# Kernel tuning notes

Measured on AMD Instinct MI355X. Metric: run time of the kernel, lower is better.

The kernel has to match this reference:

```python
import jax, jax.numpy as jnp
import numpy as np


def setup_inputs() -> dict:
    key = jax.random.key(0)
    k1, k2, k3, k4 = jax.random.split(key, 4)
    B, T, D, H = 512, 256, 512, 1024
    x = jax.random.normal(k1, (B, T, D), dtype=jnp.float32)
    # Glorot-ish scaling to keep tanh out of full saturation
    W = jax.random.normal(k2, (D, H), dtype=jnp.float32) / np.sqrt(D)
    U = jax.random.normal(k3, (H, H), dtype=jnp.float32) / np.sqrt(H)
    b = jnp.zeros((H,), dtype=jnp.float32)
    Wd = jax.random.normal(k4, (H, 1), dtype=jnp.float32) / np.sqrt(H)
    bd = jnp.zeros((1,), dtype=jnp.float32)
    return {"x": x, "W": W, "U": U, "b": b, "Wd": Wd, "bd": bd}


def reference(x, W, U, b, Wd, bd):
    # SimpleRNN: h_t = tanh(x_t @ W + h_{t-1} @ U + b), zero initial state.
    B, T, D = x.shape
    H = U.shape[0]
    # Precompute input projections for all timesteps in one big GEMM.
    xw = jnp.einsum('btd,dh->bth', x, W) + b  # [B, T, H]

    def step(h, xw_t):
        h_new = jnp.tanh(xw_t + h @ U)
        return h_new, None

    h0 = jnp.zeros((B, H), dtype=x.dtype)
    h_last, _ = jax.lax.scan(step, h0, jnp.swapaxes(xw, 0, 1))  # scan over T
    # Dense(1) on the last hidden state
    logits = h_last @ Wd + bd  # [B, 1]
    return logits
```

## Files before the change

kernel.cpp:

```cpp
#include <hip/hip_runtime.h>
#include <hip/hip_fp16.h>

#define NB 512
#define NTT 256
#define ND 512
#define NH 1024
#define NK 1536

typedef _Float16 f16;
typedef f16 f16x8 __attribute__((ext_vector_type(8)));
typedef f16 f16x4 __attribute__((ext_vector_type(4)));
typedef float f32x4 __attribute__((ext_vector_type(4)));

union U16x8 { unsigned long long q[2]; f16x8 v; uint4 u4; };
union U16x4 { unsigned long long q; f16x4 v; };

#define BAR_BYTES 4096
#define WUT_OFF  BAR_BYTES
#define WUT_BYTES (NH * NK * 2)
#define H_OFF    (WUT_OFF + WUT_BYTES)
#define H_BYTES  (2 * NB * NH * 2)

__global__ void prep_wut(const float* __restrict__ W, const float* __restrict__ U,
                         f16* __restrict__ WUT) {
    __shared__ float tile[64][65];
    int bk = blockIdx.x % 24, bn = blockIdx.x / 24;
    int k0 = bk * 64, n0 = bn * 64;
    int tid = threadIdx.x, jn = tid & 63;
#pragma unroll
    for (int p = 0; p < 16; ++p) {
        int kr = p * 4 + (tid >> 6);
        int k = k0 + kr;
        float v = (k < ND) ? W[(size_t)k * NH + n0 + jn] : U[(size_t)(k - ND) * NH + n0 + jn];
        tile[kr][jn] = v;
    }
    __syncthreads();
#pragma unroll
    for (int p = 0; p < 16; ++p) {
        int nr = p * 4 + (tid >> 6);
        int kc = tid & 63;
        WUT[(size_t)(n0 + nr) * NK + k0 + kc] = (f16)tile[kc][nr];
    }
}

__device__ __forceinline__ float fast_tanh(float x) {
    float e = __expf(-2.0f * x);
    return 2.0f / (1.0f + e) - 1.0f;
}

__global__ void __launch_bounds__(512, 1)
rnn4(const float* __restrict__ x, const f16* __restrict__ WUT,
     const float* __restrict__ bias, const float* __restrict__ Wd,
     const float* __restrict__ bd, f16* __restrict__ h,
     unsigned* __restrict__ bar, float* __restrict__ out) {
    __shared__ float red[4][64][36];
    __shared__ f16 trans[32][72];

    const int bid = blockIdx.x, tid = threadIdx.x;
    const int lane = tid & 63, wid = tid >> 6;
    const int lrow = lane & 15, lq = lane >> 4;
    const int xcd = bid & 7, m8 = bid >> 3;
    const int cl = xcd * 2 + (m8 >> 4);
    const int mem = m8 & 15;
    const int r0 = cl * 32, c0 = mem * 64;
    const int kx0 = wid * 64;
    const int kh0 = wid * 128;
    unsigned* cnt = bar + cl * 32;

    const int ec = wid * 8 + (lane & 7);
    const int eq = lane >> 3;
    const float bias_e = bias[c0 + ec];

    const int srow = tid >> 4, sseg = tid & 15;

    f16x8 bw[4][6];
#pragma unroll
    for (int j = 0; j < 4; ++j) {
        const int col = c0 + j * 16 + lrow;
        const f16* wp = WUT + (size_t)col * NK;
#pragma unroll
        for (int kt = 0; kt < 2; ++kt)
            bw[j][kt] = *(const f16x8*)(wp + kx0 + kt * 32 + lq * 8);
#pragma unroll
        for (int kt = 0; kt < 4; ++kt)
            bw[j][2 + kt] = *(const f16x8*)(wp + ND + kh0 + kt * 32 + lq * 8);
    }

    float4 xf[2][2][2];
#pragma unroll
    for (int m = 0; m < 2; ++m) {
        const float* xp = x + (size_t)(r0 + m * 16 + lrow) * (NTT * ND)
                            + kx0 + lq * 8;
#pragma unroll
        for (int kt = 0; kt < 2; ++kt) {
            xf[m][kt][0] = *(const float4*)(xp + kt * 32);
            xf[m][kt][1] = *(const float4*)(xp + kt * 32 + 4);
        }
    }

    for (int t = 0; t < NTT; ++t) {
        const f16* hprev = h + (size_t)(t & 1) * (NB * NH);
        f16* hnew = h + (size_t)((t + 1) & 1) * (NB * NH);

        f16x8 ax[2][2];
#pragma unroll
        for (int m = 0; m < 2; ++m)
#pragma unroll
            for (int kt = 0; kt < 2; ++kt) {
                const float4 a = xf[m][kt][0], b = xf[m][kt][1];
                f16x8 v = {(f16)a.x, (f16)a.y, (f16)a.z, (f16)a.w,
                           (f16)b.x, (f16)b.y, (f16)b.z, (f16)b.w};
                ax[m][kt] = v;
            }

        f32x4 acc[2][4] = {};
#pragma unroll
        for (int kt = 0; kt < 2; ++kt)
#pragma unroll
            for (int m = 0; m < 2; ++m)
#pragma unroll
                for (int j = 0; j < 4; ++j)
                    acc[m][j] = __builtin_amdgcn_mfma_f32_16x16x32_f16(ax[m][kt], bw[j][kt], acc[m][j], 0, 0, 0);

        {
            const unsigned want = (unsigned)t;
            while (__hip_atomic_load(cnt + 2 * wid,     __ATOMIC_RELAXED, __HIP_MEMORY_SCOPE_AGENT) < want ||
                   __hip_atomic_load(cnt + 2 * wid + 1, __ATOMIC_RELAXED, __HIP_MEMORY_SCOPE_AGENT) < want)
                __builtin_amdgcn_s_sleep(1);
            __builtin_amdgcn_sched_barrier(0);
        }

#pragma unroll
        for (int kt = 0; kt < 4; ++kt) {
            U16x8 a0, a1;
            const f16* p0 = hprev + (size_t)(r0 + lrow) * NH + kh0 + kt * 32 + lq * 8;
            const f16* p1 = p0 + (size_t)16 * NH;
            a0.q[0] = __hip_atomic_load((const unsigned long long*)p0, __ATOMIC_RELAXED, __HIP_MEMORY_SCOPE_AGENT);
            a0.q[1] = __hip_atomic_load((const unsigned long long*)p0 + 1, __ATOMIC_RELAXED, __HIP_MEMORY_SCOPE_AGENT);
            a1.q[0] = __hip_atomic_load((const unsigned long long*)p1, __ATOMIC_RELAXED, __HIP_MEMORY_SCOPE_AGENT);
            a1.q[1] = __hip_atomic_load((const unsigned long long*)p1 + 1, __ATOMIC_RELAXED, __HIP_MEMORY_SCOPE_AGENT);
#pragma unroll
            for (int j = 0; j < 4; ++j) {
                acc[0][j] = __builtin_amdgcn_mfma_f32_16x16x32_f16(a0.v, bw[j][2 + kt], acc[0][j], 0, 0, 0);
                acc[1][j] = __builtin_amdgcn_mfma_f32_16x16x32_f16(a1.v, bw[j][2 + kt], acc[1][j], 0, 0, 0);
            }
        }

        const int tn = (t + 1 < NTT) ? t + 1 : NTT - 1;
#pragma unroll
        for (int m = 0; m < 2; ++m) {
            const float* xp = x + (size_t)(r0 + m * 16 + lrow) * (NTT * ND)
                                + (size_t)tn * ND + kx0 + lq * 8;
#pragma unroll
            for (int kt = 0; kt < 2; ++kt) {
                xf[m][kt][0] = *(const float4*)(xp + kt * 32);
                xf[m][kt][1] = *(const float4*)(xp + kt * 32 + 4);
            }
        }

#define ST_PARTIAL(B)                                                          \
        {                                                                      \
            _Pragma("unroll")                                                  \
            for (int m = 0; m < 2; ++m)                                        \
                _Pragma("unroll")                                              \
                for (int j = 0; j < 4; ++j)                                    \
                    *(f32x4*)&red[B][j * 16 + lrow][m * 16 + lq * 4] = acc[m][j]; \
        }
#define ADD_PARTIAL(B)                                                         \
        {                                                                      \
            _Pragma("unroll")                                                  \
            for (int m = 0; m < 2; ++m)                                        \
                _Pragma("unroll")                                              \
                for (int j = 0; j < 4; ++j)                                    \
                    acc[m][j] += *(const f32x4*)&red[B][j * 16 + lrow][m * 16 + lq * 4]; \
        }
        if (wid >= 4) ST_PARTIAL(wid - 4);
        __syncthreads();
        if (wid < 4) {
            ADD_PARTIAL(wid);
            ST_PARTIAL(wid);
        }
        __syncthreads();

        {
            f32x4 s = *(const f32x4*)&red[0][ec][eq * 4];
#pragma unroll
            for (int b = 1; b < 4; ++b)
                s += *(const f32x4*)&red[b][ec][eq * 4];
#pragma unroll
            for (int r = 0; r < 4; ++r)
                trans[eq * 4 + r][ec] = (f16)fast_tanh(s[r] + bias_e);
        }
        __syncthreads();

        {
            U16x4 u;
            u.v = *(const f16x4*)&trans[srow][sseg * 4];
            __hip_atomic_store((unsigned long long*)(hnew + (size_t)(r0 + srow) * NH + c0 + sseg * 4),
                               u.q, __ATOMIC_RELAXED, __HIP_MEMORY_SCOPE_AGENT);
        }

        __syncthreads();
        if (tid == 0)
            __hip_atomic_store(cnt + mem, (unsigned)(t + 1), __ATOMIC_RELAXED, __HIP_MEMORY_SCOPE_AGENT);
    }

    if (mem == 0) {
        if (tid < 16) {
            while (__hip_atomic_load(cnt + tid, __ATOMIC_RELAXED, __HIP_MEMORY_SCOPE_AGENT) < (unsigned)NTT)
                __builtin_amdgcn_s_sleep(1);
        }
        __syncthreads();
        __builtin_amdgcn_sched_barrier(0);

        const f16* hlast = h;
        const int r = tid >> 4, seg = tid & 15;
        const f16* hp = hlast + (size_t)(r0 + r) * NH + seg * 64;
        const float* wp = Wd + seg * 64;
        float s = 0.f;
#pragma unroll
        for (int i = 0; i < 64; i += 8) {
            U16x8 u;
            u.q[0] = __hip_atomic_load((const unsigned long long*)(hp + i), __ATOMIC_RELAXED, __HIP_MEMORY_SCOPE_AGENT);
            u.q[1] = __hip_atomic_load((const unsigned long long*)(hp + i) + 1, __ATOMIC_RELAXED, __HIP_MEMORY_SCOPE_AGENT);
            const float4 w0 = *(const float4*)(wp + i);
            const float4 w1 = *(const float4*)(wp + i + 4);
            s += (float)u.v[0] * w0.x + (float)u.v[1] * w0.y +
                 (float)u.v[2] * w0.z + (float)u.v[3] * w0.w +
                 (float)u.v[4] * w1.x + (float)u.v[5] * w1.y +
                 (float)u.v[6] * w1.z + (float)u.v[7] * w1.w;
        }
        s += __shfl_xor(s, 1); s += __shfl_xor(s, 2);
        s += __shfl_xor(s, 4); s += __shfl_xor(s, 8);
        if (seg == 0) out[r0 + r] = s + bd[0];
    }
}

extern "C" void kernel_launch(void* const* d_in, const int* in_sizes, int n_in,
                              void* d_out, int out_size, void* d_ws, size_t ws_size,
                              hipStream_t stream) {
    const float* x  = (const float*)d_in[0];
    const float* W  = (const float*)d_in[1];
    const float* U  = (const float*)d_in[2];
    const float* b  = (const float*)d_in[3];
    const float* Wd = (const float*)d_in[4];
    const float* bd = (const float*)d_in[5];
    float* out = (float*)d_out;

    char* ws = (char*)d_ws;
    unsigned* bar = (unsigned*)ws;
    f16* WUT = (f16*)(ws + WUT_OFF);
    f16* h   = (f16*)(ws + H_OFF);

    hipMemsetAsync(bar, 0, BAR_BYTES, stream);
    hipMemsetAsync(h, 0, NB * NH * 2, stream);
    prep_wut<<<dim3(384), dim3(256), 0, stream>>>(W, U, WUT);

    void* args[8] = {(void*)&x, (void*)&WUT, (void*)&b, (void*)&Wd,
                     (void*)&bd, (void*)&h, (void*)&bar, (void*)&out};
    hipError_t err = hipLaunchCooperativeKernel(
        reinterpret_cast<const void*>(&rnn4), dim3(256), dim3(512), args, 0, stream);
    if (err != hipSuccess) {
        rnn4<<<dim3(256), dim3(512), 0, stream>>>(x, WUT, b, Wd, bd, h, bar, out);
    }
}
```

Before: 2.007 ms.

## Split each timestep into two 16-row halves with separate sync flags

```diff
diff --git a/kernel.cpp b/kernel.cpp
--- a/kernel.cpp
+++ b/kernel.cpp
@@ -13,7 +13,6 @@
 typedef float f32x4 __attribute__((ext_vector_type(4)));
 
 union U16x8 { unsigned long long q[2]; f16x8 v; uint4 u4; };
-union U16x4 { unsigned long long q; f16x4 v; };
 
 #define BAR_BYTES 4096
 #define WUT_OFF  BAR_BYTES
@@ -49,12 +48,12 @@
 }
 
 __global__ void __launch_bounds__(512, 1)
-rnn4(const float* __restrict__ x, const f16* __restrict__ WUT,
+rnn5(const float* __restrict__ x, const f16* __restrict__ WUT,
      const float* __restrict__ bias, const float* __restrict__ Wd,
      const float* __restrict__ bd, f16* __restrict__ h,
      unsigned* __restrict__ bar, float* __restrict__ out) {
-    __shared__ float red[4][64][36];
-    __shared__ f16 trans[32][72];
+    __shared__ float red[8][64][21];
+    __shared__ f16 trans[16][72];
 
     const int bid = blockIdx.x, tid = threadIdx.x;
     const int lane = tid & 63, wid = tid >> 6;
@@ -65,13 +64,13 @@
     const int r0 = cl * 32, c0 = mem * 64;
     const int kx0 = wid * 64;
     const int kh0 = wid * 128;
-    unsigned* cnt = bar + cl * 32;
-
-    const int ec = wid * 8 + (lane & 7);
-    const int eq = lane >> 3;
+    unsigned* flg = bar + cl * 64;
+
+    const int ec = tid & 63;
+    const int er = (tid >> 6) * 2;
     const float bias_e = bias[c0 + ec];
 
-    const int srow = tid >> 4, sseg = tid & 15;
+    const int srow = tid >> 5, sseg = tid & 31;
 
     f16x8 bw[4][6];
 #pragma unroll
@@ -88,127 +87,102 @@
 
     float4 xf[2][2][2];
 #pragma unroll
-    for (int m = 0; m < 2; ++m) {
-        const float* xp = x + (size_t)(r0 + m * 16 + lrow) * (NTT * ND)
+    for (int c = 0; c < 2; ++c) {
+        const float* xp = x + (size_t)(r0 + c * 16 + lrow) * (NTT * ND)
                             + kx0 + lq * 8;
 #pragma unroll
         for (int kt = 0; kt < 2; ++kt) {
-            xf[m][kt][0] = *(const float4*)(xp + kt * 32);
-            xf[m][kt][1] = *(const float4*)(xp + kt * 32 + 4);
+            xf[c][kt][0] = *(const float4*)(xp + kt * 32);
+            xf[c][kt][1] = *(const float4*)(xp + kt * 32 + 4);
         }
     }
 
     for (int t = 0; t < NTT; ++t) {
         const f16* hprev = h + (size_t)(t & 1) * (NB * NH);
         f16* hnew = h + (size_t)((t + 1) & 1) * (NB * NH);
-
-        f16x8 ax[2][2];
-#pragma unroll
-        for (int m = 0; m < 2; ++m)
+        const int tn = (t + 1 < NTT) ? t + 1 : NTT - 1;
+
+#pragma unroll
+        for (int c = 0; c < 2; ++c) {
+            unsigned* f = flg + c * 32;
+
+            f16x8 ax[2];
 #pragma unroll
             for (int kt = 0; kt < 2; ++kt) {
-                const float4 a = xf[m][kt][0], b = xf[m][kt][1];
+                const float4 a = xf[c][kt][0], b = xf[c][kt][1];
                 f16x8 v = {(f16)a.x, (f16)a.y, (f16)a.z, (f16)a.w,
                            (f16)b.x, (f16)b.y, (f16)b.z, (f16)b.w};
-                ax[m][kt] = v;
-            }
-
-        f32x4 acc[2][4] = {};
-#pragma unroll
-        for (int kt = 0; kt < 2; ++kt)
-#pragma unroll
-            for (int m = 0; m < 2; ++m)
+                ax[kt] = v;
+            }
+
+            f32x4 acc[4] = {};
+#pragma unroll
+            for (int kt = 0; kt < 2; ++kt)
 #pragma unroll
                 for (int j = 0; j < 4; ++j)
-                    acc[m][j] = __builtin_amdgcn_mfma_f32_16x16x32_f16(ax[m][kt], bw[j][kt], acc[m][j], 0, 0, 0);
-
-        {
-            const unsigned want = (unsigned)t;
-            while (__hip_atomic_load(cnt + 2 * wid,     __ATOMIC_RELAXED, __HIP_MEMORY_SCOPE_AGENT) < want ||
-                   __hip_atomic_load(cnt + 2 * wid + 1, __ATOMIC_RELAXED, __HIP_MEMORY_SCOPE_AGENT) < want)
-                __builtin_amdgcn_s_sleep(1);
-            __builtin_amdgcn_sched_barrier(0);
-        }
-
-#pragma unroll
-        for (int kt = 0; kt < 4; ++kt) {
-            U16x8 a0, a1;
-            const f16* p0 = hprev + (size_t)(r0 + lrow) * NH + kh0 + kt * 32 + lq * 8;
-            const f16* p1 = p0 + (size_t)16 * NH;
-            a0.q[0] = __hip_atomic_load((const unsigned long long*)p0, __ATOMIC_RELAXED, __HIP_MEMORY_SCOPE_AGENT);
-            a0.q[1] = __hip_atomic_load((const unsigned long long*)p0 + 1, __ATOMIC_RELAXED, __HIP_MEMORY_SCOPE_AGENT);
-            a1.q[0] = __hip_atomic_load((const unsigned long long*)p1, __ATOMIC_RELAXED, __HIP_MEMORY_SCOPE_AGENT);
-            a1.q[1] = __hip_atomic_load((const unsigned long long*)p1 + 1, __ATOMIC_RELAXED, __HIP_MEMORY_SCOPE_AGENT);
-#pragma unroll
-            for (int j = 0; j < 4; ++j) {
-                acc[0][j] = __builtin_amdgcn_mfma_f32_16x16x32_f16(a0.v, bw[j][2 + kt], acc[0][j], 0, 0, 0);
-                acc[1][j] = __builtin_amdgcn_mfma_f32_16x16x32_f16(a1.v, bw[j][2 + kt], acc[1][j], 0, 0, 0);
-            }
-        }
-
-        const int tn = (t + 1 < NTT) ? t + 1 : NTT - 1;
-#pragma unroll
-        for (int m = 0; m < 2; ++m) {
-            const float* xp = x + (size_t)(r0 + m * 16 + lrow) * (NTT * ND)
-                                + (size_t)tn * ND + kx0 + lq * 8;
-#pragma unroll
-            for (int kt = 0; kt < 2; ++kt) {
-                xf[m][kt][0] = *(const float4*)(xp + kt * 32);
-                xf[m][kt][1] = *(const float4*)(xp + kt * 32 + 4);
-            }
-        }
-
-#define ST_PARTIAL(B)                                                          \
-        {                                                                      \
-            _Pragma("unroll")                                                  \
-            for (int m = 0; m < 2; ++m)                                        \
-                _Pragma("unroll")                                              \
-                for (int j = 0; j < 4; ++j)                                    \
-                    *(f32x4*)&red[B][j * 16 + lrow][m * 16 + lq * 4] = acc[m][j]; \
-        }
-#define ADD_PARTIAL(B)                                                         \
-        {                                                                      \
-            _Pragma("unroll")                                                  \
-            for (int m = 0; m < 2; ++m)                                        \
-                _Pragma("unroll")                                              \
-                for (int j = 0; j < 4; ++j)                                    \
-                    acc[m][j] += *(const f32x4*)&red[B][j * 16 + lrow][m * 16 + lq * 4]; \
-        }
-        if (wid >= 4) ST_PARTIAL(wid - 4);
-        __syncthreads();
-        if (wid < 4) {
-            ADD_PARTIAL(wid);
-            ST_PARTIAL(wid);
-        }
-        __syncthreads();
-
-        {
-            f32x4 s = *(const f32x4*)&red[0][ec][eq * 4];
-#pragma unroll
-            for (int b = 1; b < 4; ++b)
-                s += *(const f32x4*)&red[b][ec][eq * 4];
-#pragma unroll
-            for (int r = 0; r < 4; ++r)
-                trans[eq * 4 + r][ec] = (f16)fast_tanh(s[r] + bias_e);
-        }
-        __syncthreads();
-
-        {
-            U16x4 u;
-            u.v = *(const f16x4*)&trans[srow][sseg * 4];
-            __hip_atomic_store((unsigned long long*)(hnew + (size_t)(r0 + srow) * NH + c0 + sseg * 4),
-                               u.q, __ATOMIC_RELAXED, __HIP_MEMORY_SCOPE_AGENT);
-        }
-
-        __syncthreads();
-        if (tid == 0)
-            __hip_atomic_store(cnt + mem, (unsigned)(t + 1), __ATOMIC_RELAXED, __HIP_MEMORY_SCOPE_AGENT);
+                    acc[j] = __builtin_amdgcn_mfma_f32_16x16x32_f16(ax[kt], bw[j][kt], acc[j], 0, 0, 0);
+
+            {
+                const unsigned want = (unsigned)t;
+                while (__hip_atomic_load(f + 2 * wid,     __ATOMIC_RELAXED, __HIP_MEMORY_SCOPE_AGENT) < want ||
+                       __hip_atomic_load(f + 2 * wid + 1, __ATOMIC_RELAXED, __HIP_MEMORY_SCOPE_AGENT) < want) {}
+                __builtin_amdgcn_sched_barrier(0);
+            }
+
+#pragma unroll
+            for (int kt = 0; kt < 4; ++kt) {
+                U16x8 a0;
+                const f16* p0 = hprev + (size_t)(r0 + c * 16 + lrow) * NH + kh0 + kt * 32 + lq * 8;
+                a0.q[0] = __hip_atomic_load((const unsigned long long*)p0, __ATOMIC_RELAXED, __HIP_MEMORY_SCOPE_AGENT);
+                a0.q[1] = __hip_atomic_load((const unsigned long long*)p0 + 1, __ATOMIC_RELAXED, __HIP_MEMORY_SCOPE_AGENT);
+#pragma unroll
+                for (int j = 0; j < 4; ++j)
+                    acc[j] = __builtin_amdgcn_mfma_f32_16x16x32_f16(a0.v, bw[j][2 + kt], acc[j], 0, 0, 0);
+            }
+
+            {
+                const float* xp = x + (size_t)(r0 + c * 16 + lrow) * (NTT * ND)
+                                    + (size_t)tn * ND + kx0 + lq * 8;
+#pragma unroll
+                for (int kt = 0; kt < 2; ++kt) {
+                    xf[c][kt][0] = *(const float4*)(xp + kt * 32);
+                    xf[c][kt][1] = *(const float4*)(xp + kt * 32 + 4);
+                }
+            }
+
+#pragma unroll
+            for (int j = 0; j < 4; ++j)
+                *(f32x4*)&red[wid][j * 16 + lrow][lq * 4] = acc[j];
+            __syncthreads();
+
+            {
+                float s0 = 0.f, s1 = 0.f;
+#pragma unroll
+                for (int b = 0; b < 8; ++b) {
+                    const float2 v = *(const float2*)&red[b][ec][er];
+                    s0 += v.x; s1 += v.y;
+                }
+                trans[er][ec]     = (f16)fast_tanh(s0 + bias_e);
+                trans[er + 1][ec] = (f16)fast_tanh(s1 + bias_e);
+            }
+            __syncthreads();
+
+            {
+                const unsigned uval = *(const unsigned*)&trans[srow][sseg * 2];
+                __hip_atomic_store((unsigned*)(hnew + (size_t)(r0 + c * 16 + srow) * NH + c0 + sseg * 2),
+                                   uval, __ATOMIC_RELAXED, __HIP_MEMORY_SCOPE_AGENT);
+            }
+
+            __syncthreads();
+            if (tid == 0)
+                __hip_atomic_store(f + mem, (unsigned)(t + 1), __ATOMIC_RELAXED, __HIP_MEMORY_SCOPE_AGENT);
+        }
     }
 
     if (mem == 0) {
-        if (tid < 16) {
-            while (__hip_atomic_load(cnt + tid, __ATOMIC_RELAXED, __HIP_MEMORY_SCOPE_AGENT) < (unsigned)NTT)
-                __builtin_amdgcn_s_sleep(1);
+        if (tid < 32) {
+            unsigned* fp = flg + (tid >> 4) * 32 + (tid & 15);
+            while (__hip_atomic_load(fp, __ATOMIC_RELAXED, __HIP_MEMORY_SCOPE_AGENT) < (unsigned)NTT) {}
         }
         __syncthreads();
         __builtin_amdgcn_sched_barrier(0);
@@ -259,8 +233,8 @@
     void* args[8] = {(void*)&x, (void*)&WUT, (void*)&b, (void*)&Wd,
                      (void*)&bd, (void*)&h, (void*)&bar, (void*)&out};
     hipError_t err = hipLaunchCooperativeKernel(
-        reinterpret_cast<const void*>(&rnn4), dim3(256), dim3(512), args, 0, stream);
+        reinterpret_cast<const void*>(&rnn5), dim3(256), dim3(512), args, 0, stream);
     if (err != hipSuccess) {
-        rnn4<<<dim3(256), dim3(512), 0, stream>>>(x, WUT, b, Wd, bd, h, bar, out);
-    }
-}
+        rnn5<<<dim3(256), dim3(512), 0, stream>>>(x, WUT, b, Wd, bd, h, bar, out);
+    }
+}
```

Result: no change. 2.026 ms (+0.9%).
